# Optimization experiments

Measured on AMD Instinct MI355X. Metric: run time of the kernel, lower is better.

The kernel has to match this reference:

```python
import jax, jax.numpy as jnp
import numpy as np

B, L, D, O = 4, 2048, 4096, 4096   # batch, seq, in_features, out_features
P = 2                               # n_pack
NF = 2000                           # n_frequency
NFP = NF // P                       # frequencies per pack
IN_P, OUT_P = D // P, O // P        # per-pack spectrum grid
NGATE = P * D // 10                 # gate parameter count
SCALING = 150.0


def setup_inputs() -> dict:
    key = jax.random.key(0)
    ks = jax.random.split(key, 6)
    x = jax.random.normal(ks[0], (B, L, D), dtype=jnp.float32)
    base_w = jax.random.normal(ks[1], (O, D), dtype=jnp.float32) * 0.02
    base_b = jax.random.normal(ks[2], (O,), dtype=jnp.float32) * 0.02
    spectrum = jax.random.normal(ks[3], (P, NFP), dtype=jnp.float32)
    B_list = jax.random.normal(ks[4], (P, P, P), dtype=jnp.float32) * 0.5
    gate_param = jax.random.normal(ks[5], (NGATE,), dtype=jnp.float32)
    # unique random frequency locations per pack (mirrors torch.randperm)
    rng = np.random.default_rng(777)
    idx = jnp.asarray(np.stack([rng.permutation(OUT_P * IN_P)[:NFP] for _ in range(P)]), dtype=jnp.int64)
    gidx = jnp.asarray(rng.permutation(P * D)[:NGATE], dtype=jnp.int64)
    return {"x": x, "base_w": base_w, "base_b": base_b, "spectrum": spectrum,
            "B_list": B_list, "gate_param": gate_param, "idx": idx, "gidx": gidx}


def _delta_weight(spec_i, idx_i, B_i, dtype):
    # scatter sparse spectrum into (OUT_P, IN_P) grid
    dense = jnp.zeros((OUT_P, IN_P), dtype).at[idx_i // IN_P, idx_i % IN_P].set(spec_i)
    A = jnp.fft.ifft2(dense).real  # (OUT_P, IN_P)
    # kron(A, B_i) -> (O, D)
    return SCALING * (A[:, None, :, None] * B_i[None, :, None, :]).reshape(O, D)


def reference(x, base_w, base_b, spectrum, B_list, gate_param, idx, gidx):
    dt = x.dtype
    # base linear
    result = jnp.einsum('bld,od->blo', x, base_w) + base_b
    # gate matrix: scatter then ifft2
    gate_m = jnp.zeros((P, D), dt).at[gidx // D, gidx % D].set(gate_param)
    gate_m = jnp.fft.ifft2(gate_m).real  # (P, D)
    gate_w = jax.nn.softmax(jnp.einsum('bld,ed->ble', x, gate_m), axis=-1)  # (B,L,P)
    # per-pack delta weights and outputs
    deltas = jax.vmap(lambda s, i, b: _delta_weight(s, i, b, dt))(spectrum, idx, B_list)  # (P,O,D)
    outputs = jnp.einsum('bld,pod->blpo', x, deltas)  # (B,L,P,O)
    final = jnp.einsum('blpo,blp->blo', outputs, gate_w)
    return (result + final).astype(dt)
```

## Files before the change

### kernel.cpp

```cpp
#include <hip/hip_runtime.h>


#define AS1 __attribute__((address_space(1)))
#define AS3 __attribute__((address_space(3)))

using bf16x8   = __attribute__((ext_vector_type(8))) __bf16;
using f32x4    = __attribute__((ext_vector_type(4))) float;
using ushort8v = __attribute__((ext_vector_type(8))) unsigned short;
using ushort4v = __attribute__((ext_vector_type(4))) unsigned short;

__device__ __forceinline__ unsigned short f2bf(float f) {
  unsigned int u = __float_as_uint(f);
  u += 0x7FFFu + ((u >> 16) & 1u);
  return (unsigned short)(u >> 16);
}

__device__ __forceinline__ void gll16(void* lds, const void* g) {
  __builtin_amdgcn_global_load_lds((AS1 void*)(g), (AS3 void*)(lds), 16, 0, 0);
}

__global__ void k_gatem(const float* __restrict__ gp, const int* __restrict__ gidx,
                        float* __restrict__ gatem, int NG) {
  int t = blockIdx.x * 256 + threadIdx.x;
  int e = t >> 12, d = t & 4095;
  float acc = 0.f;
  for (int k = 0; k < NG; k++) {
    int iv = gidx[k];
    int dk = iv & 4095;
    float th = (float)((d * dk) & 4095) * 1.5339807878856412e-3f;
    float cv = __cosf(th);
    float v = gp[k] * cv;
    acc += ((e & (iv >> 12)) & 1) ? -v : v;
  }
  gatem[t] = acc * (1.f / 8192.f);
}

__global__ void k_tables(const float* __restrict__ spec, const int* __restrict__ idx,
                         unsigned short* __restrict__ tbl, int NFP) {
  int z = blockIdx.y;
  int p = z >> 1, isQ = z & 1;
  int t = blockIdx.x * 256 + threadIdx.x;
  int r = t >> 11, kk = t & 2047;
  unsigned short v = 0;
  if (kk < 2 * NFP) {
    int j = (kk < NFP) ? kk : kk - NFP;
    int iv = idx[p * NFP + j];
    int f = isQ ? (iv & 2047) : (iv >> 11);
    float th = (float)((r * f) & 2047) * 3.0679615757712823e-3f;
    float val = (kk < NFP) ? __cosf(th) : __sinf(th);
    if (isQ) {
      float s = spec[p * NFP + j];
      val *= (kk < NFP) ? s : -s;
    }
    v = f2bf(val);
  }
  tbl[(size_t)z * 4194304 + t] = v;
}

__global__ void k_gate(const float* __restrict__ x, const float* __restrict__ gatem,
                       float* __restrict__ g) {
  int n = blockIdx.x * 4 + (threadIdx.x >> 6);
  int l = threadIdx.x & 63;
  const float4* xr  = (const float4*)(x + (size_t)n * 4096);
  const float4* g0p = (const float4*)(gatem);
  const float4* g1p = (const float4*)(gatem + 4096);
  float s0 = 0.f, s1 = 0.f;
  for (int t = 0; t < 16; t++) {
    int ii = l + (t << 6);
    float4 xv = xr[ii], a = g0p[ii], b = g1p[ii];
    s0 += xv.x * a.x + xv.y * a.y + xv.z * a.z + xv.w * a.w;
    s1 += xv.x * b.x + xv.y * b.y + xv.z * b.z + xv.w * b.w;
  }
  for (int off = 32; off > 0; off >>= 1) {
    s0 += __shfl_down(s0, off);
    s1 += __shfl_down(s1, off);
  }
  if (l == 0) {
    float mx = fmaxf(s0, s1);
    float e0 = __expf(s0 - mx), e1 = __expf(s1 - mx);
    float inv = 1.f / (e0 + e1);
    g[2 * n] = e0 * inv;
    g[2 * n + 1] = e1 * inv;
  }
}

__global__ void k_convx(const float* __restrict__ x, unsigned short* __restrict__ xb,
                        unsigned short* __restrict__ Zg, const float* __restrict__ Bl,
                        const float* __restrict__ g) {
  size_t t = (size_t)blockIdx.x * 256 + threadIdx.x;
  const float4* xp = (const float4*)x + t * 2;
  float4 v0 = xp[0], v1 = xp[1];
  ushort8v xv;
  xv[0]=f2bf(v0.x); xv[1]=f2bf(v0.y); xv[2]=f2bf(v0.z); xv[3]=f2bf(v0.w);
  xv[4]=f2bf(v1.x); xv[5]=f2bf(v1.y); xv[6]=f2bf(v1.z); xv[7]=f2bf(v1.w);
  *(ushort8v*)(xb + t * 8) = xv;
  int n = (int)(t >> 9);
  int c0 = ((int)t & 511) * 4;
  float gg[2] = {g[2 * n], g[2 * n + 1]};
  float xe[4] = {v0.x, v0.z, v1.x, v1.z};
  float xo[4] = {v0.y, v0.w, v1.y, v1.w};
  #pragma unroll
  for (int pa = 0; pa < 4; pa++) {
    int p = pa >> 1, a = pa & 1;
    float b0 = Bl[pa * 2] * gg[p], b1 = Bl[pa * 2 + 1] * gg[p];
    ushort4v yv;
    #pragma unroll
    for (int c = 0; c < 4; c++) yv[c] = f2bf(b0 * xe[c] + b1 * xo[c]);
    *(ushort4v*)(Zg + (size_t)a * 33554432 + (size_t)n * 4096 + p * 2048 + c0) = yv;
  }
}

__global__ void k_convw(const float* __restrict__ w, unsigned short* __restrict__ wb) {
  size_t t = (size_t)blockIdx.x * 256 + threadIdx.x;
  const float4* sp = (const float4*)w + t * 2;
  float4 v0 = sp[0], v1 = sp[1];
  ushort8v o;
  o[0]=f2bf(v0.x); o[1]=f2bf(v0.y); o[2]=f2bf(v0.z); o[3]=f2bf(v0.w);
  o[4]=f2bf(v1.x); o[5]=f2bf(v1.y); o[6]=f2bf(v1.z); o[7]=f2bf(v1.w);
  *(ushort8v*)(wb + t * 8) = o;
}

__device__ __forceinline__ void gemm_core(
    const unsigned short* __restrict__ Amat, int lda,
    const unsigned short* __restrict__ Bmat, int ldb,
    int K, char* As, char* Bs, f32x4 acc[4][4]) {
  const int tid = threadIdx.x;
  const int w = tid >> 6, l = tid & 63;
  const int quad = l >> 4, l15 = l & 15;
  const int wm = (w >> 1) << 6, wn = (w & 1) << 6;

  int c1 = (w << 6) + l, c2 = c1 + 256;
  int r1 = c1 >> 2, q1 = (c1 & 3) ^ ((r1 >> 1) & 3);
  int r2 = c2 >> 2, q2 = (c2 & 3) ^ ((r2 >> 1) & 3);
  const unsigned short* aS1 = Amat + (size_t)r1 * lda + (q1 << 3);
  const unsigned short* aS2 = Amat + (size_t)r2 * lda + (q2 << 3);
  const unsigned short* bS1 = Bmat + (size_t)r1 * ldb + (q1 << 3);
  const unsigned short* bS2 = Bmat + (size_t)r2 * ldb + (q2 << 3);
  char* aD1 = As + (w << 10);
  char* aD2 = As + 4096 + (w << 10);
  char* bD1 = Bs + (w << 10);
  char* bD2 = Bs + 4096 + (w << 10);

  int aOff[4], bOff[4];
  #pragma unroll
  for (int i = 0; i < 4; i++) {
    int ra = wm + (i << 4) + l15;
    aOff[i] = (ra << 6) + ((quad ^ ((ra >> 1) & 3)) << 4);
    int rb = wn + (i << 4) + l15;
    bOff[i] = (rb << 6) + ((quad ^ ((rb >> 1) & 3)) << 4);
  }

  for (int kt = 0; kt < K; kt += 32) {
    __syncthreads();
    gll16(aD1, aS1); gll16(aD2, aS2);
    gll16(bD1, bS1); gll16(bD2, bS2);
    __syncthreads();
    bf16x8 af[4], bfv[4];
    #pragma unroll
    for (int i = 0; i < 4; i++) af[i]  = *(const bf16x8*)(As + aOff[i]);
    #pragma unroll
    for (int j = 0; j < 4; j++) bfv[j] = *(const bf16x8*)(Bs + bOff[j]);
    #pragma unroll
    for (int i = 0; i < 4; i++)
      #pragma unroll
      for (int j = 0; j < 4; j++)
        acc[i][j] = __builtin_amdgcn_mfma_f32_16x16x32_bf16(af[i], bfv[j], acc[i][j], 0, 0, 0);
    aS1 += 32; aS2 += 32; bS1 += 32; bS2 += 32;
  }
}

__global__ __launch_bounds__(256, 2) void k_abuild(
    const unsigned short* __restrict__ tbl, unsigned short* __restrict__ Acat) {
  __shared__ __align__(16) char sm[16384];
  const int p = blockIdx.z;
  const unsigned short* P = tbl + (size_t)(2 * p) * 4194304;
  const unsigned short* Q = tbl + (size_t)(2 * p + 1) * 4194304;
  f32x4 acc[4][4];
  #pragma unroll
  for (int i = 0; i < 4; i++)
    #pragma unroll
    for (int j = 0; j < 4; j++) acc[i][j] = (f32x4){0.f, 0.f, 0.f, 0.f};
  const int m0 = blockIdx.x << 7, n0 = blockIdx.y << 7;
  gemm_core(P + (size_t)m0 * 2048, 2048, Q + (size_t)n0 * 2048, 2048, 2048,
            sm, sm + 8192, acc);
  const int tid = threadIdx.x, w = tid >> 6, l = tid & 63;
  const int quad = l >> 4, l15 = l & 15;
  const int wm = (w >> 1) << 6, wn = (w & 1) << 6;
  const float SC = 150.f / 4194304.f;
  unsigned short* Ap = Acat + (size_t)p * 2048;
  #pragma unroll
  for (int j = 0; j < 4; j++) {
    int c = n0 + wn + (j << 4) + l15;
    #pragma unroll
    for (int i = 0; i < 4; i++) {
      int rb = m0 + wm + (i << 4) + (quad << 2);
      #pragma unroll
      for (int reg = 0; reg < 4; reg++)
        Ap[(size_t)(rb + reg) * 4096 + c] = f2bf(acc[i][j][reg] * SC);
    }
  }
}

__device__ __forceinline__ void gemm256(const unsigned short* __restrict__ Ap,
                                        const unsigned short* __restrict__ Bp,
                                        char* sm, f32x4 acc[8][4]) {
  const int tid = threadIdx.x;
  const int wid = tid >> 6, lane = tid & 63;
  const int quad = lane >> 4, l15 = lane & 15;
  const int wr = wid >> 2, wc = wid & 3;
  const int srow = tid >> 2, g = tid & 3;
  const int q = g ^ ((srow >> 1) & 3);
  const size_t soff = (size_t)srow * 4096 + (size_t)(q << 3);
  const int slotx = (quad ^ ((l15 >> 1) & 3)) << 4;
  const int aB = (((wr << 7) + l15) << 6) + slotx;
  const int bB = (((wc << 6) + l15) << 6) + slotx + 16384;

#define STG(BUF, ISB, RR, KT)                                                  \
  gll16(sm + (BUF) * 32768 + (ISB) * 16384 + (RR) * 8192 + (wid << 10),        \
        ((ISB) ? Bp : Ap) + soff + (size_t)(RR) * 524288 + (KT))

  STG(0, 0, 0, 0);  STG(0, 0, 1, 0);
  STG(0, 1, 0, 0);  STG(0, 1, 1, 0);
  STG(1, 0, 0, 32); STG(1, 0, 1, 32);
  asm volatile("s_waitcnt vmcnt(2)" ::: "memory");
  __builtin_amdgcn_s_barrier();

  bf16x8 af[8], bfv[4];
  for (int it = 0; it < 64; it++) {
    const int kt = it << 6;
    const bool pref = (it < 63);
    #pragma unroll
    for (int i = 0; i < 8; i++) af[i]  = *(const bf16x8*)(sm + aB + i * 1024);
    #pragma unroll
    for (int j = 0; j < 4; j++) bfv[j] = *(const bf16x8*)(sm + bB + j * 1024);
    STG(1, 1, 0, kt + 32); STG(1, 1, 1, kt + 32);
    asm volatile("s_waitcnt lgkmcnt(0)" ::: "memory");
    __builtin_amdgcn_s_setprio(1);
    #pragma unroll
    for (int i = 0; i < 4; i++)
      #pragma unroll
      for (int j = 0; j < 4; j++)
        acc[i][j] = __builtin_amdgcn_mfma_f32_16x16x32_bf16(af[i], bfv[j], acc[i][j], 0, 0, 0);
    __builtin_amdgcn_s_setprio(0);
    __builtin_amdgcn_s_barrier();
    if (pref) { STG(0, 0, 0, kt + 64); STG(0, 0, 1, kt + 64); }
    __builtin_amdgcn_s_setprio(1);
    #pragma unroll
    for (int i = 4; i < 8; i++)
      #pragma unroll
      for (int j = 0; j < 4; j++)
        acc[i][j] = __builtin_amdgcn_mfma_f32_16x16x32_bf16(af[i], bfv[j], acc[i][j], 0, 0, 0);
    __builtin_amdgcn_s_setprio(0);
    if (pref) asm volatile("s_waitcnt vmcnt(2)" ::: "memory");
    else      asm volatile("s_waitcnt vmcnt(0)" ::: "memory");
    __builtin_amdgcn_s_barrier();
    #pragma unroll
    for (int i = 0; i < 8; i++) af[i]  = *(const bf16x8*)(sm + 32768 + aB + i * 1024);
    #pragma unroll
    for (int j = 0; j < 4; j++) bfv[j] = *(const bf16x8*)(sm + 32768 + bB + j * 1024);
    if (pref) { STG(0, 1, 0, kt + 64); STG(0, 1, 1, kt + 64); }
    asm volatile("s_waitcnt lgkmcnt(0)" ::: "memory");
    __builtin_amdgcn_s_setprio(1);
    #pragma unroll
    for (int i = 0; i < 4; i++)
      #pragma unroll
      for (int j = 0; j < 4; j++)
        acc[i][j] = __builtin_amdgcn_mfma_f32_16x16x32_bf16(af[i], bfv[j], acc[i][j], 0, 0, 0);
    __builtin_amdgcn_s_setprio(0);
    __builtin_amdgcn_s_barrier();
    if (pref) { STG(1, 0, 0, kt + 96); STG(1, 0, 1, kt + 96); }
    __builtin_amdgcn_s_setprio(1);
    #pragma unroll
    for (int i = 4; i < 8; i++)
      #pragma unroll
      for (int j = 0; j < 4; j++)
        acc[i][j] = __builtin_amdgcn_mfma_f32_16x16x32_bf16(af[i], bfv[j], acc[i][j], 0, 0, 0);
    __builtin_amdgcn_s_setprio(0);
    if (pref) asm volatile("s_waitcnt vmcnt(2)" ::: "memory");
    __builtin_amdgcn_s_barrier();
  }
#undef STG
}

__global__ __launch_bounds__(512, 2) void k_base(
    const unsigned short* __restrict__ xb, const unsigned short* __restrict__ wb,
    const float* __restrict__ bias, float* __restrict__ out) {
  __shared__ __align__(16) char sm[65536];
  int lid = blockIdx.x + (blockIdx.y << 4);
  int nl = ((lid & 7) << 6) + (lid >> 3);
  const int m0 = (nl >> 4) << 8, n0 = (nl & 15) << 8;
  f32x4 acc[8][4];
  #pragma unroll
  for (int i = 0; i < 8; i++)
    #pragma unroll
    for (int j = 0; j < 4; j++) acc[i][j] = (f32x4){0.f, 0.f, 0.f, 0.f};
  gemm256(xb + (size_t)m0 * 4096, wb + (size_t)n0 * 4096, sm, acc);
  const int tid = threadIdx.x, wid = tid >> 6, lane = tid & 63;
  const int quad = lane >> 4, l15 = lane & 15;
  const int wr = wid >> 2, wc = wid & 3;
  #pragma unroll
  for (int j = 0; j < 4; j++) {
    int o = n0 + (wc << 6) + (j << 4) + l15;
    float bv = bias[o];
    #pragma unroll
    for (int i = 0; i < 8; i++) {
      int mb = m0 + (wr << 7) + (i << 4) + (quad << 2);
      #pragma unroll
      for (int reg = 0; reg < 4; reg++)
        out[(size_t)(mb + reg) * 4096 + o] = acc[i][j][reg] + bv;
    }
  }
}

__global__ __launch_bounds__(512, 2) void k_pack(
    const unsigned short* __restrict__ Zg, const unsigned short* __restrict__ Acat,
    float* __restrict__ out) {
  __shared__ __align__(16) char sm[65536];
  int lid = blockIdx.x + (blockIdx.y << 3);
  int nl = ((lid & 7) << 6) + (lid >> 3);
  const int bx = nl & 7, by = nl >> 3;
  const int a = by & 1, nt = by >> 1;
  const int r0 = bx << 8;
  f32x4 acc[8][4];
  #pragma unroll
  for (int i = 0; i < 8; i++)
    #pragma unroll
    for (int j = 0; j < 4; j++) acc[i][j] = (f32x4){0.f, 0.f, 0.f, 0.f};
  gemm256(Zg + ((size_t)(a << 13) + (size_t)(nt << 8)) * 4096,
          Acat + (size_t)r0 * 4096, sm, acc);
  const int tid = threadIdx.x, wid = tid >> 6, lane = tid & 63;
  const int quad = lane >> 4, l15 = lane & 15;
  const int wr = wid >> 2, wc = wid & 3;
  #pragma unroll
  for (int j = 0; j < 4; j++) {
    int r = r0 + (wc << 6) + (j << 4) + l15;
    #pragma unroll
    for (int i = 0; i < 8; i++) {
      int nb = (nt << 8) + (wr << 7) + (i << 4) + (quad << 2);
      #pragma unroll
      for (int reg = 0; reg < 4; reg++) {
        float* p = out + (size_t)(nb + reg) * 4096 + 2 * r + a;
        *p += acc[i][j][reg];
      }
    }
  }
}

extern "C" void kernel_launch(void* const* d_in, const int* in_sizes, int n_in,
                              void* d_out, int out_size, void* d_ws, size_t ws_size,
                              hipStream_t stream) {
  const float* x    = (const float*)d_in[0];
  const float* basw = (const float*)d_in[1];
  const float* basb = (const float*)d_in[2];
  const float* spec = (const float*)d_in[3];
  const float* Bl   = (const float*)d_in[4];
  const float* gp   = (const float*)d_in[5];
  const int*   idx  = (const int*)d_in[6];
  const int*   gidx = (const int*)d_in[7];
  const int NFP = in_sizes[3] / 2;
  const int NG  = in_sizes[5];

  char* ws = (char*)d_ws;
  float*          gbuf  = (float*)(ws);
  float*          gatem = (float*)(ws + (64ull << 10));
  unsigned short* Acat  = (unsigned short*)(ws + (1ull << 20));
  unsigned short* xb    = (unsigned short*)(ws + (32ull << 20));
  unsigned short* bwb   = (unsigned short*)(ws + (96ull << 20));
  unsigned short* Zg    = (unsigned short*)(ws + (128ull << 20));
  unsigned short* tbl   = (unsigned short*)(ws + (128ull << 20));
  float* outp = (float*)d_out;

  k_gatem <<<32, 256, 0, stream>>>(gp, gidx, gatem, NG);
  k_tables<<<dim3(16384, 4), 256, 0, stream>>>(spec, idx, tbl, NFP);
  k_abuild<<<dim3(16, 16, 2), 256, 0, stream>>>(tbl, Acat);
  k_gate  <<<2048, 256, 0, stream>>>(x, gatem, gbuf);
  k_convx <<<16384, 256, 0, stream>>>(x, xb, Zg, Bl, gbuf);
  k_convw <<<8192, 256, 0, stream>>>(basw, bwb);
  k_base  <<<dim3(16, 32), 512, 0, stream>>>(xb, bwb, basb, outp);
  k_pack  <<<dim3(8, 64), 512, 0, stream>>>(Zg, Acat, outp);
  (void)n_in; (void)out_size; (void)ws_size;
}
```

Before: 1.004 ms.

## Use four-stage LDS ring buffer in bf16 GEMM with one block per CU

Replaces the double-buffered 256x256 GEMM mainloop with a four-buffer (128 KB LDS) ring that prefetches three K-tiles ahead. A and B tile loads are split across the two half-steps. Both GEMM kernels now request 128 KB shared memory and launch bounds of one block per CU. The deeper prefetch is meant to hide global-load latency better, at the cost of halving occupancy, which removes inter-block latency hiding.

```diff
diff --git a/kernel.cpp b/kernel.cpp
--- a/kernel.cpp
+++ b/kernel.cpp
@@ -201,9 +201,57 @@
   }
 }
 
+
+__device__ __forceinline__ void stg_unit(char* sm, const unsigned short* base,
+                                         size_t soff, int wid, int buf, int isb,
+                                         int kt) {
+  char* d = sm + buf * 32768 + isb * 16384 + (wid << 10);
+  gll16(d,        base + soff + kt);
+  gll16(d + 8192, base + soff + 524288 + kt);
+}
+
+__device__ __forceinline__ void tile_step(
+    char* sm, const unsigned short* __restrict__ Ap,
+    const unsigned short* __restrict__ Bp, size_t soff,
+    int aB, int bB, int wid, f32x4 (&acc)[8][4], int T, bool do_stg, int vm) {
+  bf16x8 af[8], bfv[4];
+  char* bb = sm + (T & 3) * 32768;
+  #pragma unroll
+  for (int i = 0; i < 4; i++) af[i]  = *(const bf16x8*)(bb + aB + i * 1024);
+  #pragma unroll
+  for (int j = 0; j < 4; j++) bfv[j] = *(const bf16x8*)(bb + bB + j * 1024);
+  if (do_stg) stg_unit(sm, Ap, soff, wid, (T + 3) & 3, 0, (T + 3) << 5);
+  __builtin_amdgcn_s_barrier();
+  asm volatile("s_waitcnt lgkmcnt(0)" ::: "memory");
+  __builtin_amdgcn_s_setprio(1);
+  #pragma unroll
+  for (int i = 0; i < 4; i++)
+    #pragma unroll
+    for (int j = 0; j < 4; j++)
+      acc[i][j] = __builtin_amdgcn_mfma_f32_16x16x32_bf16(af[i], bfv[j], acc[i][j], 0, 0, 0);
+  __builtin_amdgcn_s_setprio(0);
+  __builtin_amdgcn_s_barrier();
+  #pragma unroll
+  for (int i = 4; i < 8; i++) af[i] = *(const bf16x8*)(bb + aB + i * 1024);
+  if (do_stg) stg_unit(sm, Bp, soff, wid, (T + 3) & 3, 1, (T + 3) << 5);
+  __builtin_amdgcn_s_barrier();
+  asm volatile("s_waitcnt lgkmcnt(0)" ::: "memory");
+  __builtin_amdgcn_s_setprio(1);
+  #pragma unroll
+  for (int i = 4; i < 8; i++)
+    #pragma unroll
+    for (int j = 0; j < 4; j++)
+      acc[i][j] = __builtin_amdgcn_mfma_f32_16x16x32_bf16(af[i], bfv[j], acc[i][j], 0, 0, 0);
+  __builtin_amdgcn_s_setprio(0);
+  if (vm == 8)      asm volatile("s_waitcnt vmcnt(8)" ::: "memory");
+  else if (vm == 4) asm volatile("s_waitcnt vmcnt(4)" ::: "memory");
+  else              asm volatile("s_waitcnt vmcnt(0)" ::: "memory");
+  __builtin_amdgcn_s_barrier();
+}
+
 __device__ __forceinline__ void gemm256(const unsigned short* __restrict__ Ap,
                                         const unsigned short* __restrict__ Bp,
-                                        char* sm, f32x4 acc[8][4]) {
+                                        char* sm, f32x4 (&acc)[8][4]) {
   const int tid = threadIdx.x;
   const int wid = tid >> 6, lane = tid & 63;
   const int quad = lane >> 4, l15 = lane & 15;
@@ -215,77 +263,27 @@
   const int aB = (((wr << 7) + l15) << 6) + slotx;
   const int bB = (((wc << 6) + l15) << 6) + slotx + 16384;
 
-#define STG(BUF, ISB, RR, KT)                                                  \
-  gll16(sm + (BUF) * 32768 + (ISB) * 16384 + (RR) * 8192 + (wid << 10),        \
-        ((ISB) ? Bp : Ap) + soff + (size_t)(RR) * 524288 + (KT))
-
-  STG(0, 0, 0, 0);  STG(0, 0, 1, 0);
-  STG(0, 1, 0, 0);  STG(0, 1, 1, 0);
-  STG(1, 0, 0, 32); STG(1, 0, 1, 32);
-  asm volatile("s_waitcnt vmcnt(2)" ::: "memory");
-  __builtin_amdgcn_s_barrier();
-
-  bf16x8 af[8], bfv[4];
-  for (int it = 0; it < 64; it++) {
-    const int kt = it << 6;
-    const bool pref = (it < 63);
-    #pragma unroll
-    for (int i = 0; i < 8; i++) af[i]  = *(const bf16x8*)(sm + aB + i * 1024);
-    #pragma unroll
-    for (int j = 0; j < 4; j++) bfv[j] = *(const bf16x8*)(sm + bB + j * 1024);
-    STG(1, 1, 0, kt + 32); STG(1, 1, 1, kt + 32);
-    asm volatile("s_waitcnt lgkmcnt(0)" ::: "memory");
-    __builtin_amdgcn_s_setprio(1);
-    #pragma unroll
-    for (int i = 0; i < 4; i++)
-      #pragma unroll
-      for (int j = 0; j < 4; j++)
-        acc[i][j] = __builtin_amdgcn_mfma_f32_16x16x32_bf16(af[i], bfv[j], acc[i][j], 0, 0, 0);
-    __builtin_amdgcn_s_setprio(0);
-    __builtin_amdgcn_s_barrier();
-    if (pref) { STG(0, 0, 0, kt + 64); STG(0, 0, 1, kt + 64); }
-    __builtin_amdgcn_s_setprio(1);
-    #pragma unroll
-    for (int i = 4; i < 8; i++)
-      #pragma unroll
-      for (int j = 0; j < 4; j++)
-        acc[i][j] = __builtin_amdgcn_mfma_f32_16x16x32_bf16(af[i], bfv[j], acc[i][j], 0, 0, 0);
-    __builtin_amdgcn_s_setprio(0);
-    if (pref) asm volatile("s_waitcnt vmcnt(2)" ::: "memory");
-    else      asm volatile("s_waitcnt vmcnt(0)" ::: "memory");
-    __builtin_amdgcn_s_barrier();
-    #pragma unroll
-    for (int i = 0; i < 8; i++) af[i]  = *(const bf16x8*)(sm + 32768 + aB + i * 1024);
-    #pragma unroll
-    for (int j = 0; j < 4; j++) bfv[j] = *(const bf16x8*)(sm + 32768 + bB + j * 1024);
-    if (pref) { STG(0, 1, 0, kt + 64); STG(0, 1, 1, kt + 64); }
-    asm volatile("s_waitcnt lgkmcnt(0)" ::: "memory");
-    __builtin_amdgcn_s_setprio(1);
-    #pragma unroll
-    for (int i = 0; i < 4; i++)
-      #pragma unroll
-      for (int j = 0; j < 4; j++)
-        acc[i][j] = __builtin_amdgcn_mfma_f32_16x16x32_bf16(af[i], bfv[j], acc[i][j], 0, 0, 0);
-    __builtin_amdgcn_s_setprio(0);
-    __builtin_amdgcn_s_barrier();
-    if (pref) { STG(1, 0, 0, kt + 96); STG(1, 0, 1, kt + 96); }
-    __builtin_amdgcn_s_setprio(1);
-    #pragma unroll
-    for (int i = 4; i < 8; i++)
-      #pragma unroll
-      for (int j = 0; j < 4; j++)
-        acc[i][j] = __builtin_amdgcn_mfma_f32_16x16x32_bf16(af[i], bfv[j], acc[i][j], 0, 0, 0);
-    __builtin_amdgcn_s_setprio(0);
-    if (pref) asm volatile("s_waitcnt vmcnt(2)" ::: "memory");
-    __builtin_amdgcn_s_barrier();
-  }
-#undef STG
-}
-
-__global__ __launch_bounds__(512, 2) void k_base(
+  stg_unit(sm, Ap, soff, wid, 0, 0, 0);
+  stg_unit(sm, Bp, soff, wid, 0, 1, 0);
+  stg_unit(sm, Ap, soff, wid, 1, 0, 32);
+  stg_unit(sm, Bp, soff, wid, 1, 1, 32);
+  stg_unit(sm, Ap, soff, wid, 2, 0, 64);
+  stg_unit(sm, Bp, soff, wid, 2, 1, 64);
+  asm volatile("s_waitcnt vmcnt(8)" ::: "memory");
+  __builtin_amdgcn_s_barrier();
+
+  #pragma unroll 4
+  for (int t = 0; t < 125; t++)
+    tile_step(sm, Ap, Bp, soff, aB, bB, wid, acc, t, true, 8);
+  tile_step(sm, Ap, Bp, soff, aB, bB, wid, acc, 125, false, 4);
+  tile_step(sm, Ap, Bp, soff, aB, bB, wid, acc, 126, false, 0);
+  tile_step(sm, Ap, Bp, soff, aB, bB, wid, acc, 127, false, 0);
+}
+
+__global__ __launch_bounds__(512, 1) void k_base(
     const unsigned short* __restrict__ xb, const unsigned short* __restrict__ wb,
     const float* __restrict__ bias, float* __restrict__ out) {
-  __shared__ __align__(16) char sm[65536];
+  __shared__ __align__(16) char sm[131072];
   int lid = blockIdx.x + (blockIdx.y << 4);
   int nl = ((lid & 7) << 6) + (lid >> 3);
   const int m0 = (nl >> 4) << 8, n0 = (nl & 15) << 8;
@@ -312,10 +310,10 @@
   }
 }
 
-__global__ __launch_bounds__(512, 2) void k_pack(
+__global__ __launch_bounds__(512, 1) void k_pack(
     const unsigned short* __restrict__ Zg, const unsigned short* __restrict__ Acat,
     float* __restrict__ out) {
-  __shared__ __align__(16) char sm[65536];
+  __shared__ __align__(16) char sm[131072];
   int lid = blockIdx.x + (blockIdx.y << 3);
   int nl = ((lid & 7) << 6) + (lid >> 3);
   const int bx = nl & 7, by = nl >> 3;
```

New measurement: 1.002 ms. Within noise of the previous version (-0.2%).
